# Optimization experiments

Measured on AMD Instinct MI355X. Metric: run time of the kernel, lower is better.

## Reference

```python
import jax, jax.numpy as jnp
import numpy as np

BLOCK = 32  # GGUF Q8_0 block size
O, I = 4096, 4096
NB = I // BLOCK  # blocks per output row
B, S = 2, 2048


def setup_inputs() -> dict:
    key = jax.random.key(0)
    k1, k2, k3, k4 = jax.random.split(key, 4)
    x = jax.random.normal(k1, (B, S, I), dtype=jnp.float32)
    # signed int8 quants stored as int32 (values in [-128, 127])
    q_weight = jax.random.randint(k2, (O, I), 0, 256, dtype=jnp.int32) - 128
    # per-block fp scales (small positive, as produced by Q8_0 quantization)
    scales = jax.random.uniform(k3, (O, NB), dtype=jnp.float32) * 0.02 + 1e-4
    bias = jax.random.normal(k4, (O,), dtype=jnp.float32)
    return {"x": x, "q_weight": q_weight, "scales": scales, "bias": bias}


def dequantize(q_weight, scales, dtype):
    # q_weight: [O, I] int, scales: [O, NB] float; block-wise dequant (Q8_0)
    q = q_weight.reshape(O, NB, BLOCK).astype(dtype)
    w = q * scales.astype(dtype)[:, :, None]
    return w.reshape(O, I)  # [O, I]


def reference(x, q_weight, scales, bias):
    # cast_bias_weight: dequantize weight/bias to the input dtype, then linear
    dtype = x.dtype
    w = dequantize(q_weight, scales, dtype)          # [O, I]
    y = jnp.einsum('bsi,oi->bso', x, w) + bias.astype(dtype)
    return y
```

## Files before the change

kernel.cpp:

```cpp
#include <hip/hip_runtime.h>
#include <hip/hip_bf16.h>
#include <stdint.h>


#define M_DIM 4096
#define N_DIM 4096
#define K_DIM 4096
#define NB_SC 128

#define BM 256
#define BN 256
#define BKB 128
#define NT (K_DIM / BKB)
#define TILE_B (BM * BKB)

typedef __attribute__((ext_vector_type(4))) int i32x4;

__device__ __forceinline__ void gload_lds16(const void* gsrc, void* ldsdst) {
  __builtin_amdgcn_global_load_lds(
      (__attribute__((address_space(1))) void*)(uintptr_t)gsrc,
      (__attribute__((address_space(3))) void*)(uint32_t)(uintptr_t)ldsdst,
      16, 0, 0);
}

__device__ __forceinline__ int pack4(int a, int b, int c, int d) {
  return (a & 255) | ((b & 255) << 8) | ((c & 255) << 16) | ((d & 255) << 24);
}


__global__ void prep_kernel(const float* __restrict__ x, const int* __restrict__ q,
                            const float* __restrict__ sc,
                            char* __restrict__ xb, char* __restrict__ wb,
                            float* __restrict__ sxv, float* __restrict__ swv) {
  __shared__ float red[4];
  const int b = blockIdx.x;
  const int t = threadIdx.x;
  if (b < 4096) {
    const float4* row = (const float4*)(x + (size_t)b * K_DIM);
    float4 v[4];
    float m = 0.f;
#pragma unroll
    for (int i = 0; i < 4; ++i) {
      v[i] = row[t * 4 + i];
      m = fmaxf(m, fmaxf(fmaxf(fabsf(v[i].x), fabsf(v[i].y)),
                         fmaxf(fabsf(v[i].z), fabsf(v[i].w))));
    }
#pragma unroll
    for (int off = 32; off >= 1; off >>= 1) m = fmaxf(m, __shfl_xor(m, off, 64));
    if ((t & 63) == 0) red[t >> 6] = m;
    __syncthreads();
    m = fmaxf(fmaxf(red[0], red[1]), fmaxf(red[2], red[3]));
    const float inv = (m > 0.f) ? 127.0f / m : 0.f;
    int4 o;
    o.x = pack4(__float2int_rn(v[0].x * inv), __float2int_rn(v[0].y * inv),
                __float2int_rn(v[0].z * inv), __float2int_rn(v[0].w * inv));
    o.y = pack4(__float2int_rn(v[1].x * inv), __float2int_rn(v[1].y * inv),
                __float2int_rn(v[1].z * inv), __float2int_rn(v[1].w * inv));
    o.z = pack4(__float2int_rn(v[2].x * inv), __float2int_rn(v[2].y * inv),
                __float2int_rn(v[2].z * inv), __float2int_rn(v[2].w * inv));
    o.w = pack4(__float2int_rn(v[3].x * inv), __float2int_rn(v[3].y * inv),
                __float2int_rn(v[3].z * inv), __float2int_rn(v[3].w * inv));
    ((int4*)(xb + (size_t)b * K_DIM))[t] = o;
    if (t == 0) sxv[b] = m / 127.0f;
  } else {
    const int o_row = b - 4096;
    float m = sc[o_row * NB_SC + (t & 127)];
#pragma unroll
    for (int off = 32; off >= 1; off >>= 1) m = fmaxf(m, __shfl_xor(m, off, 64));
    if ((t & 63) == 0) red[t >> 6] = m;
    __syncthreads();
    m = fmaxf(fmaxf(red[0], red[1]), fmaxf(red[2], red[3]));
    const float ratio = sc[o_row * NB_SC + (t >> 1)] / m;
    const int4* qp = (const int4*)(q + (size_t)o_row * K_DIM);
    int4 qv[4];
#pragma unroll
    for (int i = 0; i < 4; ++i) qv[i] = qp[t * 4 + i];
    int4 ov;
    ov.x = pack4(__float2int_rn((float)qv[0].x * ratio), __float2int_rn((float)qv[0].y * ratio),
                 __float2int_rn((float)qv[0].z * ratio), __float2int_rn((float)qv[0].w * ratio));
    ov.y = pack4(__float2int_rn((float)qv[1].x * ratio), __float2int_rn((float)qv[1].y * ratio),
                 __float2int_rn((float)qv[1].z * ratio), __float2int_rn((float)qv[1].w * ratio));
    ov.z = pack4(__float2int_rn((float)qv[2].x * ratio), __float2int_rn((float)qv[2].y * ratio),
                 __float2int_rn((float)qv[2].z * ratio), __float2int_rn((float)qv[2].w * ratio));
    ov.w = pack4(__float2int_rn((float)qv[3].x * ratio), __float2int_rn((float)qv[3].y * ratio),
                 __float2int_rn((float)qv[3].z * ratio), __float2int_rn((float)qv[3].w * ratio));
    ((int4*)(wb + (size_t)o_row * K_DIM))[t] = ov;
    if (t == 0) swv[o_row] = m;
  }
}


__device__ __forceinline__ i32x4 lds_frag(const char* t, int r, int kb) {
  return *(const i32x4*)(t + r * BKB + ((((kb) >> 4) ^ (r & 7)) << 4));
}

__device__ __forceinline__ void stage_half(const char* __restrict__ pX,
                                           char* lds, int hr0, int ktb, int w) {
#pragma unroll
  for (int j = 0; j < 2; ++j) {
    gload_lds16(pX + (size_t)(hr0 + j * 8) * K_DIM + ktb,
                lds + (hr0 + w * 16 + j * 8) * BKB);
  }
}

__device__ __forceinline__ void read_a(const char* Ac, int r0, int frow, int fkb,
                                       i32x4 (&af)[2][2]) {
#pragma unroll
  for (int q = 0; q < 2; ++q)
#pragma unroll
    for (int kk = 0; kk < 2; ++kk)
      af[q][kk] = lds_frag(Ac, r0 + q * 16 + frow, kk * 64 + fkb);
}

__device__ __forceinline__ void read_b(const char* Bc, int wn, int frow, int fkb,
                                       i32x4 (&bf)[4][2]) {
#pragma unroll
  for (int ni = 0; ni < 4; ++ni)
#pragma unroll
    for (int kk = 0; kk < 2; ++kk)
      bf[ni][kk] = lds_frag(Bc, wn * 64 + ni * 16 + frow, kk * 64 + fkb);
}

__device__ __forceinline__ void mfma_quad(const i32x4 (&af)[2][2], const i32x4 (&bf)[4][2],
                                          i32x4 (&acc)[8][4], int q0) {
  __builtin_amdgcn_s_setprio(1);
#pragma unroll
  for (int q = 0; q < 2; ++q)
#pragma unroll
    for (int ni = 0; ni < 4; ++ni)
#pragma unroll
      for (int kk = 0; kk < 2; ++kk)
        acc[q0 + q][ni] =
            __builtin_amdgcn_mfma_i32_16x16x64_i8(af[q][kk], bf[ni][kk], acc[q0 + q][ni], 0, 0, 0);
  __builtin_amdgcn_s_setprio(0);
}

template <int BUF, int MODE>
__device__ __forceinline__ void ktile(const char* __restrict__ pA,
                                      const char* __restrict__ pB,
                                      char* AsB, char* BsB,
                                      int ktb, int w, int wm, int wn, int frow, int fkb,
                                      i32x4 (&acc)[8][4],
                                      i32x4 (&bf_cur)[4][2], i32x4 (&bf_nxt)[4][2],
                                      i32x4 (&a0_cur)[2][2], i32x4 (&a0_nxt)[2][2]) {
  const char* Ac = AsB + BUF * TILE_B;
  const char* An = AsB + (BUF ^ 1) * TILE_B;
  const char* Bn = BsB + (BUF ^ 1) * TILE_B;
  char* Anw = AsB + (BUF ^ 1) * TILE_B;
  char* Bw  = BsB + BUF * TILE_B;

  i32x4 a1[2][2], a2[2][2], a3[2][2];

  read_a(Ac, wm * 128 + 32, frow, fkb, a1);
  if (MODE < 2) {
    stage_half(pA, Anw, 0, ktb + BKB, w);
    stage_half(pA, Anw, 128, ktb + BKB, w);
  }
  __builtin_amdgcn_sched_barrier(0);
  mfma_quad(a0_cur, bf_cur, acc, 0);
  __builtin_amdgcn_s_barrier();

  read_a(Ac, wm * 128 + 64, frow, fkb, a2);
  if (MODE == 0) stage_half(pB, Bw, 0, ktb + 2 * BKB, w);
  __builtin_amdgcn_sched_barrier(0);
  mfma_quad(a1, bf_cur, acc, 2);
  __builtin_amdgcn_s_barrier();

  read_a(Ac, wm * 128 + 96, frow, fkb, a3);
  if (MODE == 0) stage_half(pB, Bw, 128, ktb + 2 * BKB, w);
  __builtin_amdgcn_sched_barrier(0);
  mfma_quad(a2, bf_cur, acc, 4);
  __builtin_amdgcn_s_barrier();

  if (MODE == 0)
    asm volatile("s_waitcnt vmcnt(4)" ::: "memory");
  else if (MODE == 1)
    asm volatile("s_waitcnt vmcnt(0)" ::: "memory");
  if (MODE < 2) {
    read_b(Bn, wn, frow, fkb, bf_nxt);
    read_a(An, wm * 128 + 0, frow, fkb, a0_nxt);
  }
  __builtin_amdgcn_sched_barrier(0);
  mfma_quad(a3, bf_cur, acc, 6);
  __builtin_amdgcn_s_barrier();
}

__global__ __launch_bounds__(512, 2) void gemm256(const char* __restrict__ A,
                                                  const char* __restrict__ B,
                                                  const float* __restrict__ sxv,
                                                  const float* __restrict__ swv,
                                                  const float* __restrict__ bias,
                                                  float* __restrict__ C) {
  __shared__ char AsB[2 * TILE_B];
  __shared__ char BsB[2 * TILE_B];

  const int tid = threadIdx.x;
  const int w = tid >> 6;
  const int l = tid & 63;
  const int wm = w >> 2;
  const int wn = w & 3;
  const int frow = l & 15;
  const int fkb = (l >> 4) * 16;

  const int bid = blockIdx.x;
  const int cpx = gridDim.x >> 3;
  const int swz = (bid & 7) * cpx + (bid >> 3);
  const int bm0 = (swz >> 4) * BM;
  const int bn0 = (swz & 15) * BN;

  const int sr = l >> 3;
  const int skp = ((l & 7) ^ sr) << 4;
  const char* pA = A + (size_t)(bm0 + w * 16 + sr) * K_DIM + skp;
  const char* pB = B + (size_t)(bn0 + w * 16 + sr) * K_DIM + skp;

  i32x4 acc[8][4] = {};
  i32x4 bf0[4][2], bf1[4][2];
  i32x4 a00[2][2], a01[2][2];

  stage_half(pB, BsB, 0, 0, w);
  stage_half(pB, BsB, 128, 0, w);
  stage_half(pA, AsB, 0, 0, w);
  stage_half(pA, AsB, 128, 0, w);
  stage_half(pB, BsB + TILE_B, 0, BKB, w);
  stage_half(pB, BsB + TILE_B, 128, BKB, w);
  asm volatile("s_waitcnt vmcnt(4)" ::: "memory");
  __builtin_amdgcn_s_barrier();
  read_b(BsB, wn, frow, fkb, bf0);
  read_a(AsB, wm * 128 + 0, frow, fkb, a00);

  for (int t = 0; t < NT - 2; t += 2) {
    ktile<0, 0>(pA, pB, AsB, BsB, t * BKB, w, wm, wn, frow, fkb, acc, bf0, bf1, a00, a01);
    ktile<1, 0>(pA, pB, AsB, BsB, (t + 1) * BKB, w, wm, wn, frow, fkb, acc, bf1, bf0, a01, a00);
  }
  ktile<0, 1>(pA, pB, AsB, BsB, (NT - 2) * BKB, w, wm, wn, frow, fkb, acc, bf0, bf1, a00, a01);
  ktile<1, 2>(pA, pB, AsB, BsB, (NT - 1) * BKB, w, wm, wn, frow, fkb, acc, bf1, bf0, a01, a00);

#pragma unroll
  for (int ni = 0; ni < 4; ++ni) {
    const int n = bn0 + wn * 64 + ni * 16 + (l & 15);
    const float swn = swv[n];
    const float bv = bias[n];
#pragma unroll
    for (int mi = 0; mi < 8; ++mi) {
      const int mbase = bm0 + wm * 128 + mi * 16 + (l >> 4) * 4;
#pragma unroll
      for (int r = 0; r < 4; ++r)
        C[(size_t)(mbase + r) * N_DIM + n] =
            (float)acc[mi][ni][r] * (swn * sxv[mbase + r]) + bv;
    }
  }
}


__global__ void naive_kernel(const float* __restrict__ x, const int* __restrict__ q,
                             const float* __restrict__ sc, const float* __restrict__ bias,
                             float* __restrict__ out) {
  size_t idx = (size_t)blockIdx.x * blockDim.x + threadIdx.x;
  if (idx >= (size_t)M_DIM * N_DIM) return;
  int n = (int)(idx & (N_DIM - 1));
  size_t m = idx >> 12;
  float acc = 0.f;
  for (int k = 0; k < K_DIM; k += 32) {
    float s = sc[n * NB_SC + (k >> 5)];
    float part = 0.f;
    for (int j = 0; j < 32; ++j)
      part += x[m * K_DIM + k + j] * (float)q[(size_t)n * K_DIM + k + j];
    acc += part * s;
  }
  out[idx] = acc + bias[n];
}


extern "C" void kernel_launch(void* const* d_in, const int* in_sizes, int n_in,
                              void* d_out, int out_size, void* d_ws, size_t ws_size,
                              hipStream_t stream) {
  const float* x    = (const float*)d_in[0];
  const int*   q    = (const int*)d_in[1];
  const float* sc   = (const float*)d_in[2];
  const float* bias = (const float*)d_in[3];
  float* out = (float*)d_out;

  const size_t elems = (size_t)M_DIM * K_DIM;
  const size_t need  = 2 * elems + 2 * 4096 * sizeof(float);

  if (ws_size >= need) {
    char* xb = (char*)d_ws;
    char* wb = xb + elems;
    float* sxv = (float*)(wb + elems);
    float* swv = sxv + 4096;
    hipLaunchKernelGGL(prep_kernel, dim3(8192), dim3(256), 0, stream,
                       x, q, sc, xb, wb, sxv, swv);
    hipLaunchKernelGGL(gemm256, dim3((M_DIM / BM) * (N_DIM / BN)), dim3(512), 0, stream,
                       xb, wb, sxv, swv, bias, out);
  } else {
    hipLaunchKernelGGL(naive_kernel, dim3((M_DIM * N_DIM) / 256), dim3(256), 0, stream,
                       x, q, sc, bias, out);
  }
}
```

Baseline: 91.15 us.

## Switch int8 GEMM to 32x32x32 MFMA tiles with k-slice operand reads

Replaces the 16x16x64 int8 MFMA with the 32x32x32 variant. Each wave now holds a 4x2 grid of 32x32 accumulators, and the A/B fragment reads and the epilogue row mapping are reorganized to match. The larger MFMA shape is meant to raise operand reuse per instruction and cut the number of LDS fragment reads and MFMA issues per k-tile. In exchange the pipeline is now split across k-slices instead of m-quarters, and the output layout mapping changes, which risks correctness mistakes and different register pressure.

```diff
diff --git a/kernel.cpp b/kernel.cpp
--- a/kernel.cpp
+++ b/kernel.cpp
@@ -15,6 +15,7 @@
 #define TILE_B (BM * BKB)
 
 typedef __attribute__((ext_vector_type(4))) int i32x4;
+typedef __attribute__((ext_vector_type(16))) int i32x16;
 
 __device__ __forceinline__ void gload_lds16(const void* gsrc, void* ldsdst) {
   __builtin_amdgcn_global_load_lds(
@@ -103,35 +104,32 @@
   }
 }
 
-__device__ __forceinline__ void read_a(const char* Ac, int r0, int frow, int fkb,
-                                       i32x4 (&af)[2][2]) {
-#pragma unroll
-  for (int q = 0; q < 2; ++q)
-#pragma unroll
-    for (int kk = 0; kk < 2; ++kk)
-      af[q][kk] = lds_frag(Ac, r0 + q * 16 + frow, kk * 64 + fkb);
-}
-
-__device__ __forceinline__ void read_b(const char* Bc, int wn, int frow, int fkb,
-                                       i32x4 (&bf)[4][2]) {
-#pragma unroll
-  for (int ni = 0; ni < 4; ++ni)
-#pragma unroll
-    for (int kk = 0; kk < 2; ++kk)
-      bf[ni][kk] = lds_frag(Bc, wn * 64 + ni * 16 + frow, kk * 64 + fkb);
-}
-
-__device__ __forceinline__ void mfma_quad(const i32x4 (&af)[2][2], const i32x4 (&bf)[4][2],
-                                          i32x4 (&acc)[8][4], int q0) {
+__device__ __forceinline__ void read_aks(const char* Ac, int wm, int l31, int kb,
+                                         i32x4 (&af)[4]) {
+#pragma unroll
+  for (int mt = 0; mt < 4; ++mt)
+    af[mt] = lds_frag(Ac, wm * 128 + mt * 32 + l31, kb);
+}
+
+__device__ __forceinline__ void read_ball(const char* Bc, int wn, int l31, int kbb,
+                                          i32x4 (&bf)[2][4]) {
+#pragma unroll
+  for (int nt = 0; nt < 2; ++nt)
+#pragma unroll
+    for (int ks = 0; ks < 4; ++ks)
+      bf[nt][ks] = lds_frag(Bc, wn * 64 + nt * 32 + l31, kbb + ks * 32);
+}
+
+template <int KS>
+__device__ __forceinline__ void mfma_ks(const i32x4 (&af)[4], const i32x4 (&bf)[2][4],
+                                        i32x16 (&acc)[4][2]) {
   __builtin_amdgcn_s_setprio(1);
 #pragma unroll
-  for (int q = 0; q < 2; ++q)
-#pragma unroll
-    for (int ni = 0; ni < 4; ++ni)
-#pragma unroll
-      for (int kk = 0; kk < 2; ++kk)
-        acc[q0 + q][ni] =
-            __builtin_amdgcn_mfma_i32_16x16x64_i8(af[q][kk], bf[ni][kk], acc[q0 + q][ni], 0, 0, 0);
+  for (int mt = 0; mt < 4; ++mt)
+#pragma unroll
+    for (int nt = 0; nt < 2; ++nt)
+      acc[mt][nt] =
+          __builtin_amdgcn_mfma_i32_32x32x32_i8(af[mt], bf[nt][KS], acc[mt][nt], 0, 0, 0);
   __builtin_amdgcn_s_setprio(0);
 }
 
@@ -139,37 +137,37 @@
 __device__ __forceinline__ void ktile(const char* __restrict__ pA,
                                       const char* __restrict__ pB,
                                       char* AsB, char* BsB,
-                                      int ktb, int w, int wm, int wn, int frow, int fkb,
-                                      i32x4 (&acc)[8][4],
-                                      i32x4 (&bf_cur)[4][2], i32x4 (&bf_nxt)[4][2],
-                                      i32x4 (&a0_cur)[2][2], i32x4 (&a0_nxt)[2][2]) {
+                                      int ktb, int w, int wm, int wn, int l31, int kbb,
+                                      i32x16 (&acc)[4][2],
+                                      i32x4 (&bf_cur)[2][4], i32x4 (&bf_nxt)[2][4],
+                                      i32x4 (&a0_cur)[4], i32x4 (&a0_nxt)[4]) {
   const char* Ac = AsB + BUF * TILE_B;
   const char* An = AsB + (BUF ^ 1) * TILE_B;
   const char* Bn = BsB + (BUF ^ 1) * TILE_B;
   char* Anw = AsB + (BUF ^ 1) * TILE_B;
   char* Bw  = BsB + BUF * TILE_B;
 
-  i32x4 a1[2][2], a2[2][2], a3[2][2];
-
-  read_a(Ac, wm * 128 + 32, frow, fkb, a1);
+  i32x4 a1[4], a2[4], a3[4];
+
+  read_aks(Ac, wm, l31, kbb + 32, a1);
   if (MODE < 2) {
     stage_half(pA, Anw, 0, ktb + BKB, w);
     stage_half(pA, Anw, 128, ktb + BKB, w);
   }
   __builtin_amdgcn_sched_barrier(0);
-  mfma_quad(a0_cur, bf_cur, acc, 0);
-  __builtin_amdgcn_s_barrier();
-
-  read_a(Ac, wm * 128 + 64, frow, fkb, a2);
+  mfma_ks<0>(a0_cur, bf_cur, acc);
+  __builtin_amdgcn_s_barrier();
+
+  read_aks(Ac, wm, l31, kbb + 64, a2);
   if (MODE == 0) stage_half(pB, Bw, 0, ktb + 2 * BKB, w);
   __builtin_amdgcn_sched_barrier(0);
-  mfma_quad(a1, bf_cur, acc, 2);
-  __builtin_amdgcn_s_barrier();
-
-  read_a(Ac, wm * 128 + 96, frow, fkb, a3);
+  mfma_ks<1>(a1, bf_cur, acc);
+  __builtin_amdgcn_s_barrier();
+
+  read_aks(Ac, wm, l31, kbb + 96, a3);
   if (MODE == 0) stage_half(pB, Bw, 128, ktb + 2 * BKB, w);
   __builtin_amdgcn_sched_barrier(0);
-  mfma_quad(a2, bf_cur, acc, 4);
+  mfma_ks<2>(a2, bf_cur, acc);
   __builtin_amdgcn_s_barrier();
 
   if (MODE == 0)
@@ -177,11 +175,11 @@
   else if (MODE == 1)
     asm volatile("s_waitcnt vmcnt(0)" ::: "memory");
   if (MODE < 2) {
-    read_b(Bn, wn, frow, fkb, bf_nxt);
-    read_a(An, wm * 128 + 0, frow, fkb, a0_nxt);
-  }
-  __builtin_amdgcn_sched_barrier(0);
-  mfma_quad(a3, bf_cur, acc, 6);
+    read_ball(Bn, wn, l31, kbb, bf_nxt);
+    read_aks(An, wm, l31, kbb, a0_nxt);
+  }
+  __builtin_amdgcn_sched_barrier(0);
+  mfma_ks<3>(a3, bf_cur, acc);
   __builtin_amdgcn_s_barrier();
 }
 
@@ -199,8 +197,8 @@
   const int l = tid & 63;
   const int wm = w >> 2;
   const int wn = w & 3;
-  const int frow = l & 15;
-  const int fkb = (l >> 4) * 16;
+  const int l31 = l & 31;
+  const int kbb = (l >> 5) * 16;
 
   const int bid = blockIdx.x;
   const int cpx = gridDim.x >> 3;
@@ -213,9 +211,9 @@
   const char* pA = A + (size_t)(bm0 + w * 16 + sr) * K_DIM + skp;
   const char* pB = B + (size_t)(bn0 + w * 16 + sr) * K_DIM + skp;
 
-  i32x4 acc[8][4] = {};
-  i32x4 bf0[4][2], bf1[4][2];
-  i32x4 a00[2][2], a01[2][2];
+  i32x16 acc[4][2] = {};
+  i32x4 bf0[2][4], bf1[2][4];
+  i32x4 a00[4], a01[4];
 
   stage_half(pB, BsB, 0, 0, w);
   stage_half(pB, BsB, 128, 0, w);
@@ -225,28 +223,29 @@
   stage_half(pB, BsB + TILE_B, 128, BKB, w);
   asm volatile("s_waitcnt vmcnt(4)" ::: "memory");
   __builtin_amdgcn_s_barrier();
-  read_b(BsB, wn, frow, fkb, bf0);
-  read_a(AsB, wm * 128 + 0, frow, fkb, a00);
+  read_ball(BsB, wn, l31, kbb, bf0);
+  read_aks(AsB, wm, l31, kbb, a00);
 
   for (int t = 0; t < NT - 2; t += 2) {
-    ktile<0, 0>(pA, pB, AsB, BsB, t * BKB, w, wm, wn, frow, fkb, acc, bf0, bf1, a00, a01);
-    ktile<1, 0>(pA, pB, AsB, BsB, (t + 1) * BKB, w, wm, wn, frow, fkb, acc, bf1, bf0, a01, a00);
-  }
-  ktile<0, 1>(pA, pB, AsB, BsB, (NT - 2) * BKB, w, wm, wn, frow, fkb, acc, bf0, bf1, a00, a01);
-  ktile<1, 2>(pA, pB, AsB, BsB, (NT - 1) * BKB, w, wm, wn, frow, fkb, acc, bf1, bf0, a01, a00);
-
-#pragma unroll
-  for (int ni = 0; ni < 4; ++ni) {
-    const int n = bn0 + wn * 64 + ni * 16 + (l & 15);
+    ktile<0, 0>(pA, pB, AsB, BsB, t * BKB, w, wm, wn, l31, kbb, acc, bf0, bf1, a00, a01);
+    ktile<1, 0>(pA, pB, AsB, BsB, (t + 1) * BKB, w, wm, wn, l31, kbb, acc, bf1, bf0, a01, a00);
+  }
+  ktile<0, 1>(pA, pB, AsB, BsB, (NT - 2) * BKB, w, wm, wn, l31, kbb, acc, bf0, bf1, a00, a01);
+  ktile<1, 2>(pA, pB, AsB, BsB, (NT - 1) * BKB, w, wm, wn, l31, kbb, acc, bf1, bf0, a01, a00);
+
+#pragma unroll
+  for (int nt = 0; nt < 2; ++nt) {
+    const int n = bn0 + wn * 64 + nt * 32 + l31;
     const float swn = swv[n];
     const float bv = bias[n];
 #pragma unroll
-    for (int mi = 0; mi < 8; ++mi) {
-      const int mbase = bm0 + wm * 128 + mi * 16 + (l >> 4) * 4;
-#pragma unroll
-      for (int r = 0; r < 4; ++r)
-        C[(size_t)(mbase + r) * N_DIM + n] =
-            (float)acc[mi][ni][r] * (swn * sxv[mbase + r]) + bv;
+    for (int mt = 0; mt < 4; ++mt) {
+      const int mbase = bm0 + wm * 128 + mt * 32 + (l >> 5) * 4;
+#pragma unroll
+      for (int r = 0; r < 16; ++r) {
+        const int m = mbase + (r & 3) + 8 * (r >> 2);
+        C[(size_t)m * N_DIM + n] = (float)acc[mt][nt][r] * (swn * sxv[m]) + bv;
+      }
     }
   }
 }
```

Measured after the change: 99.16 us. 1.09x slower.
